# Kernel tuning notes

Hardware: AMD Instinct MI355X
Metric: run time of the kernel (lower is better)

## Reference

```python
import jax, jax.numpy as jnp
import numpy as np

B, T, D, H = 8, 2048, 1024, 128  # batch, seq, input_size, head_size


def setup_inputs() -> dict:
    key = jax.random.key(0)
    kx, kq, kk, kv = jax.random.split(key, 4)
    s = 1.0 / np.sqrt(D)
    return {
        "x": jax.random.normal(kx, (B, T, D), dtype=jnp.float32),
        "Wq": jax.random.normal(kq, (D, H), dtype=jnp.float32) * s,
        "Wk": jax.random.normal(kk, (D, H), dtype=jnp.float32) * s,
        "Wv": jax.random.normal(kv, (D, H), dtype=jnp.float32) * s,
    }


def reference(x, Wq, Wk, Wv):
    # projections (Linear, no bias)
    q = jnp.einsum("btd,dh->bth", x, Wq)
    k = jnp.einsum("btd,dh->bth", x, Wk)
    v = jnp.einsum("btd,dh->bth", x, Wv)
    scale = H ** (-0.5)
    scores = jnp.einsum("bth,bsh->bts", q, k) * scale  # [B,T,T]
    t = x.shape[1]
    causal = jnp.tril(jnp.ones((t, t), dtype=bool))
    scores = jnp.where(causal, scores, -jnp.inf)
    attn = jax.nn.softmax(scores, axis=-1)  # dropout p=0.0 -> identity
    out = jnp.einsum("bts,bsh->bth", attn, v)
    return out
```

## Files before the change

### kernel.cpp

```cpp
#include <hip/hip_runtime.h>
#include <math.h>

#define B_ 8
#define T_ 2048
#define D_ 1024
#define H_ 128
#define BT (B_ * T_)

typedef short bf16x8 __attribute__((ext_vector_type(8)));
typedef float f32x4 __attribute__((ext_vector_type(4)));

static constexpr float SCALE = 0.08838834764831845f;

__device__ inline unsigned short f2b(float f) {
  unsigned int u = __float_as_uint(f);
  u += 0x7FFF + ((u >> 16) & 1);
  return (unsigned short)(u >> 16);
}
__device__ inline unsigned int pk2(float a, float b) {
  return (unsigned int)f2b(a) | ((unsigned int)f2b(b) << 16);
}

__device__ __forceinline__ void gll16(const void* g, void* l) {
  __builtin_amdgcn_global_load_lds(
      (const __attribute__((address_space(1))) void*)g,
      (__attribute__((address_space(3))) void*)l, 16, 0, 0);
}

__global__ __launch_bounds__(256) void wcvt_kernel(
    const float* __restrict__ Wq, const float* __restrict__ Wk,
    const float* __restrict__ Wv, short* __restrict__ Wt) {
  __shared__ short Wls[128 * 72];
  const int sel = blockIdx.y;
  const float* W = sel == 0 ? Wq : (sel == 1 ? Wk : Wv);
  const int d0 = blockIdx.x * 64;
  const int tid = threadIdx.x;
#pragma unroll
  for (int i = 0; i < 8; ++i) {
    int slot = tid + i * 256;
    int r = slot >> 5, hg = slot & 31;
    float4 w = *(const float4*)(W + (size_t)(d0 + r) * H_ + hg * 4);
    Wls[(hg * 4 + 0) * 72 + r] = (short)f2b(w.x);
    Wls[(hg * 4 + 1) * 72 + r] = (short)f2b(w.y);
    Wls[(hg * 4 + 2) * 72 + r] = (short)f2b(w.z);
    Wls[(hg * 4 + 3) * 72 + r] = (short)f2b(w.w);
  }
  __syncthreads();
  short* dst = Wt + (size_t)sel * D_ * H_;
#pragma unroll
  for (int i = 0; i < 4; ++i) {
    int slot = tid + i * 256;
    int h = slot >> 3, g = slot & 7;
    *(int4*)(dst + (size_t)h * D_ + d0 + g * 8) = *(int4*)&Wls[h * 72 + g * 8];
  }
}

__global__ __launch_bounds__(256) void proj_kernel(
    const float* __restrict__ x, const short* __restrict__ Wt,
    short* __restrict__ qb, short* __restrict__ kb, short* __restrict__ vtb) {
  __shared__ alignas(16) char smem[49152];
  short* Xs0 = (short*)smem;
  short* Xs1 = (short*)(smem + 8192);
  short* Ws0 = (short*)(smem + 16384);
  short* Ws1 = (short*)(smem + 32768);

  const int tid = threadIdx.x;
  const int wave = tid >> 6, lane = tid & 63;
  const int ln = lane & 15, quad = lane >> 4;
  const int mw = wave & 1, nw = wave >> 1;
  const int sel = blockIdx.y;
  const int row0 = blockIdx.x * 64;
  const short* W = Wt + (size_t)sel * (size_t)(D_ * H_);

  f32x4 acc[2][4];
#pragma unroll
  for (int mi = 0; mi < 2; ++mi)
#pragma unroll
    for (int ni = 0; ni < 4; ++ni) acc[mi][ni] = (f32x4){0.f, 0.f, 0.f, 0.f};

  auto stage = [&](int bf, int k0) {
    short* Ws = bf ? Ws1 : Ws0;
#pragma unroll
    for (int j = 0; j < 4; ++j) {
      const int rbase = wave * 32 + j * 8;
      const int n = rbase + (lane >> 3);
      const int gp = (lane & 7) ^ (n & 7);
      gll16(W + (size_t)n * D_ + k0 + gp * 8, (char*)Ws + rbase * 128);
    }
    short* Xs = bf ? Xs1 : Xs0;
    float4 xr[4];
#pragma unroll
    for (int i = 0; i < 4; ++i) {
      int fid = tid + i * 256;
      int r = fid >> 4, g4 = fid & 15;
      xr[i] = *(const float4*)(x + (size_t)(row0 + r) * D_ + k0 + g4 * 4);
    }
#pragma unroll
    for (int i = 0; i < 4; ++i) {
      int fid = tid + i * 256;
      int r = fid >> 4, g4 = fid & 15;
      int g = g4 >> 1, half = g4 & 1;
      unsigned int* p = (unsigned int*)&Xs[r * 64 + ((g ^ (r & 7)) * 8) + half * 4];
      p[0] = pk2(xr[i].x, xr[i].y);
      p[1] = pk2(xr[i].z, xr[i].w);
    }
  };

  stage(0, 0);
  for (int s = 0; s < 16; ++s) {
    __syncthreads();
    if (s < 15) stage((s + 1) & 1, (s + 1) * 64);
    const short* Xs = (s & 1) ? Xs1 : Xs0;
    const short* Ws = (s & 1) ? Ws1 : Ws0;
#pragma unroll
    for (int kk = 0; kk < 2; ++kk) {
      bf16x8 a[2];
#pragma unroll
      for (int mi = 0; mi < 2; ++mi) {
        int r = mw * 32 + mi * 16 + ln;
        a[mi] = *(bf16x8*)&Xs[r * 64 + (((kk * 4 + quad) ^ (r & 7)) * 8)];
      }
#pragma unroll
      for (int ni = 0; ni < 4; ++ni) {
        int n = nw * 64 + ni * 16 + ln;
        bf16x8 bb = *(bf16x8*)&Ws[n * 64 + (((kk * 4 + quad) ^ (n & 7)) * 8)];
#pragma unroll
        for (int mi = 0; mi < 2; ++mi)
          acc[mi][ni] = __builtin_amdgcn_mfma_f32_16x16x32_bf16(a[mi], bb, acc[mi][ni], 0, 0, 0);
      }
    }
  }

  __syncthreads();
  short* Cs = (short*)smem;
  if (sel < 2) {
    short* out = sel ? kb : qb;
#pragma unroll
    for (int mi = 0; mi < 2; ++mi)
#pragma unroll
      for (int ni = 0; ni < 4; ++ni)
#pragma unroll
        for (int rr = 0; rr < 4; ++rr)
          Cs[(mw * 32 + mi * 16 + quad * 4 + rr) * 136 + nw * 64 + ni * 16 + ln] =
              (short)f2b(acc[mi][ni][rr]);
    __syncthreads();
#pragma unroll
    for (int i = 0; i < 4; ++i) {
      int slot = tid + i * 256;
      int r = slot >> 4, g = slot & 15;
      *(int4*)(out + (size_t)(row0 + r) * H_ + g * 8) = *(int4*)&Cs[r * 136 + g * 8];
    }
  } else {
#pragma unroll
    for (int mi = 0; mi < 2; ++mi)
#pragma unroll
      for (int ni = 0; ni < 4; ++ni)
#pragma unroll
        for (int rr = 0; rr < 4; ++rr)
          Cs[(nw * 64 + ni * 16 + ln) * 72 + mw * 32 + mi * 16 + quad * 4 + rr] =
              (short)f2b(acc[mi][ni][rr]);
    __syncthreads();
    const int b = row0 >> 11, t0 = row0 & 2047;
#pragma unroll
    for (int i = 0; i < 4; ++i) {
      int slot = tid + i * 256;
      int h = slot >> 3, g = slot & 7;
      *(int4*)(vtb + (size_t)(b * H_ + h) * T_ + t0 + g * 8) = *(int4*)&Cs[h * 72 + g * 8];
    }
  }
}

__global__ __launch_bounds__(256) void attn_part(
    const short* __restrict__ qb, const short* __restrict__ kb,
    const short* __restrict__ vtb, float* __restrict__ po,
    float* __restrict__ pm, float* __restrict__ pl) {
  __shared__ alignas(16) char smem[74240];
  short* Ks0 = (short*)smem;
  short* Ks1 = (short*)(smem + 16384);
  short* Vt0 = (short*)(smem + 32768);
  short* Vt1 = (short*)(smem + 49152);
  short* Pt  = (short*)(smem + 65536);

  const int tid = threadIdx.x;
  const int wv = tid >> 6, lane = tid & 63;
  const int ln = lane & 15, quad = lane >> 4;
  const int b = blockIdx.x / 80;
  const int rr = 79 - (blockIdx.x % 80);
  const int g = (rr >= 48) ? 3 : (rr >= 24) ? 2 : (rr >= 8) ? 1 : 0;
  const int local = rr - 4 * g * (g + 1);
  const int j = 8 * g + local / (g + 1);
  const int s = local - (local / (g + 1)) * (g + 1);
  const int sid = b * 80 + rr;
  const int q0 = j * 64;
  const int nchunks = min(8, j + 1 - 8 * s);

  short* myP = Pt + wv * (16 * 68);

  bf16x8 qfr[4];
#pragma unroll
  for (int kk = 0; kk < 4; ++kk)
    qfr[kk] = *(const bf16x8*)(qb + (size_t)(b * T_ + q0 + wv * 16 + ln) * H_ +
                               kk * 32 + quad * 8);

  f32x4 oacc[8];
#pragma unroll
  for (int ht = 0; ht < 8; ++ht) oacc[ht] = (f32x4){0.f, 0.f, 0.f, 0.f};

  float m_run = -INFINITY, l_run = 0.f;
  const int qglob = q0 + wv * 16 + ln;

  auto stageK = [&](short* dst, int s0) {
#pragma unroll
    for (int jj = 0; jj < 4; ++jj) {
      const int rb = wv * 16 + jj * 4;
      const int r = rb + (lane >> 4);
      const int gp = (lane & 15) ^ (r & 7);
      gll16(kb + (size_t)(b * T_ + s0 + r) * H_ + gp * 8, (char*)dst + rb * 256);
    }
  };
  auto stageV = [&](short* dst, int s0) {
#pragma unroll
    for (int jj = 0; jj < 4; ++jj) {
      const int hb = wv * 32 + jj * 8;
      const int h = hb + (lane >> 3);
      const int gp = (lane & 7) ^ (h & 7);
      gll16(vtb + (size_t)(b * H_ + h) * T_ + s0 + gp * 8, (char*)dst + hb * 128);
    }
  };

  stageK(Ks0, 8 * s * 64);
  stageV(Vt0, 8 * s * 64);

  for (int ch = 0; ch < nchunks; ++ch) {
    const int s0 = (8 * s + ch) * 64;
    const int cur = ch & 1;
    __syncthreads();
    if (ch + 1 < nchunks) {
      stageK(cur ? Ks0 : Ks1, s0 + 64);
      stageV(cur ? Vt0 : Vt1, s0 + 64);
    }
    const short* Kc = cur ? Ks1 : Ks0;
    const short* Vc = cur ? Vt1 : Vt0;

    f32x4 sacc[4];
#pragma unroll
    for (int t = 0; t < 4; ++t) sacc[t] = (f32x4){0.f, 0.f, 0.f, 0.f};
#pragma unroll
    for (int kk = 0; kk < 4; ++kk) {
#pragma unroll
      for (int t = 0; t < 4; ++t) {
        const int krow = t * 16 + ln;
        bf16x8 kf = *(bf16x8*)&Kc[krow * 128 + (((kk * 4 + quad) ^ (ln & 7)) * 8)];
        sacc[t] = __builtin_amdgcn_mfma_f32_16x16x32_bf16(kf, qfr[kk], sacc[t], 0, 0, 0);
      }
    }

    float sv[4][4];
    float mc = -INFINITY;
#pragma unroll
    for (int t = 0; t < 4; ++t)
#pragma unroll
      for (int r = 0; r < 4; ++r) {
        const int key = s0 + t * 16 + quad * 4 + r;
        float sc = sacc[t][r] * SCALE;
        sv[t][r] = (key <= qglob) ? sc : -INFINITY;
        mc = fmaxf(mc, sv[t][r]);
      }
    mc = fmaxf(mc, __shfl_xor(mc, 16));
    mc = fmaxf(mc, __shfl_xor(mc, 32));
    const float mnew = fmaxf(m_run, mc);
    const float alpha = __expf(m_run - mnew);
    float lc = 0.f;
    float p[4][4];
#pragma unroll
    for (int t = 0; t < 4; ++t)
#pragma unroll
      for (int r = 0; r < 4; ++r) {
        p[t][r] = __expf(sv[t][r] - mnew);
        lc += p[t][r];
      }
    lc += __shfl_xor(lc, 16);
    lc += __shfl_xor(lc, 32);
    l_run = l_run * alpha + lc;
    m_run = mnew;

#pragma unroll
    for (int t = 0; t < 4; ++t) {
      *(unsigned int*)&myP[ln * 68 + t * 16 + quad * 4 + 0] = pk2(p[t][0], p[t][1]);
      *(unsigned int*)&myP[ln * 68 + t * 16 + quad * 4 + 2] = pk2(p[t][2], p[t][3]);
    }
#pragma unroll
    for (int ht = 0; ht < 8; ++ht)
#pragma unroll
      for (int r = 0; r < 4; ++r) oacc[ht][r] *= alpha;

#pragma unroll
    for (int kk2 = 0; kk2 < 2; ++kk2) {
      bf16x8 pf = *(bf16x8*)&myP[ln * 68 + kk2 * 32 + quad * 8];
#pragma unroll
      for (int ht = 0; ht < 8; ++ht) {
        const int hrow = ht * 16 + ln;
        bf16x8 vf = *(bf16x8*)&Vc[hrow * 64 + (((kk2 * 4 + quad) ^ (ln & 7)) * 8)];
        oacc[ht] = __builtin_amdgcn_mfma_f32_16x16x32_bf16(vf, pf, oacc[ht], 0, 0, 0);
      }
    }
  }

  if (quad == 0) {
    pm[(size_t)sid * 64 + wv * 16 + ln] = m_run;
    pl[(size_t)sid * 64 + wv * 16 + ln] = l_run;
  }
  __syncthreads();
  float* Ot = (float*)smem;
#pragma unroll
  for (int ht = 0; ht < 8; ++ht)
    *(f32x4*)&Ot[(wv * 16 + ln) * 132 + ht * 16 + quad * 4] = oacc[ht];
  __syncthreads();
  float* dst = po + (size_t)sid * 8192;
#pragma unroll
  for (int i = 0; i < 8; ++i) {
    int slot2 = tid + i * 256;
    int r2 = slot2 >> 5, c2 = slot2 & 31;
    *(f32x4*)(dst + r2 * 128 + c2 * 4) = *(f32x4*)&Ot[r2 * 132 + c2 * 4];
  }
}

__global__ __launch_bounds__(256) void attn_reduce(
    const float* __restrict__ po, const float* __restrict__ pm,
    const float* __restrict__ pl, float* __restrict__ out) {
  const int b = blockIdx.x >> 5;
  const int j = blockIdx.x & 31;
  const int g = j >> 3;
  const int nseg = g + 1;
  const int sid0 = b * 80 + 4 * g * (g + 1) + (j - 8 * g) * nseg;
  const int tid = threadIdx.x;
  const int q = tid >> 2, hq = tid & 3;

  float m[4], l[4], a[4];
  float M = -INFINITY;
  for (int s2 = 0; s2 < nseg; ++s2) {
    m[s2] = pm[(size_t)(sid0 + s2) * 64 + q];
    l[s2] = pl[(size_t)(sid0 + s2) * 64 + q];
    M = fmaxf(M, m[s2]);
  }
  float lsum = 0.f;
  for (int s2 = 0; s2 < nseg; ++s2) {
    a[s2] = __expf(m[s2] - M);
    lsum += a[s2] * l[s2];
  }
  f32x4 acc[8];
#pragma unroll
  for (int i = 0; i < 8; ++i) acc[i] = (f32x4){0.f, 0.f, 0.f, 0.f};
  for (int s2 = 0; s2 < nseg; ++s2) {
    const float* src = po + (size_t)(sid0 + s2) * 8192 + q * 128 + hq * 32;
    const float as = a[s2];
#pragma unroll
    for (int i = 0; i < 8; ++i) {
      f32x4 v = *(const f32x4*)(src + i * 4);
#pragma unroll
      for (int c = 0; c < 4; ++c) acc[i][c] += as * v[c];
    }
  }
  const float inv = 1.0f / lsum;
  float* o = out + ((size_t)(b * T_ + j * 64 + q)) * H_ + hq * 32;
#pragma unroll
  for (int i = 0; i < 8; ++i) {
    f32x4 v;
#pragma unroll
    for (int c = 0; c < 4; ++c) v[c] = acc[i][c] * inv;
    *(f32x4*)(o + i * 4) = v;
  }
}

extern "C" void kernel_launch(void* const* d_in, const int* in_sizes, int n_in,
                              void* d_out, int out_size, void* d_ws, size_t ws_size,
                              hipStream_t stream) {
  const float* x  = (const float*)d_in[0];
  const float* Wq = (const float*)d_in[1];
  const float* Wk = (const float*)d_in[2];
  const float* Wv = (const float*)d_in[3];
  float* out = (float*)d_out;

  char* ws = (char*)d_ws;
  short* qb  = (short*)(ws);
  short* kb  = (short*)(ws + 4194304);
  short* vtb = (short*)(ws + 8388608);
  short* Wt  = (short*)(ws + 12582912);
  float* po  = (float*)(ws + 14680064);
  float* pm  = (float*)(ws + 35651584);
  float* pl  = (float*)(ws + 35915776);

  wcvt_kernel<<<dim3(D_ / 64, 3), 256, 0, stream>>>(Wq, Wk, Wv, Wt);
  proj_kernel<<<dim3(BT / 64, 3), 256, 0, stream>>>(x, Wt, qb, kb, vtb);
  attn_part<<<dim3(8 * 80), 256, 0, stream>>>(qb, kb, vtb, po, pm, pl);
  attn_reduce<<<dim3(8 * 32), 256, 0, stream>>>(po, pm, pl, out);
}
```

Before: 165.4 us.

## Load K/V fragments directly from global memory and drop LDS staging in attention

Removes the double-buffered LDS staging of K and V tiles and has each wave read its MFMA operands straight from global memory, relying on L1/L2 for reuse across waves. It also reorders block indexing so batches interleave, skips the causal mask on fully-unmasked chunks, and writes partial outputs directly without an LDS transpose. The aim is to cut LDS footprint and barriers to raise occupancy. The cost is more redundant global/L2 traffic and less coalesced access (the V reads are strided by T).

```diff
diff --git a/kernel.cpp b/kernel.cpp
--- a/kernel.cpp
+++ b/kernel.cpp
@@ -174,18 +174,13 @@
     const short* __restrict__ qb, const short* __restrict__ kb,
     const short* __restrict__ vtb, float* __restrict__ po,
     float* __restrict__ pm, float* __restrict__ pl) {
-  __shared__ alignas(16) char smem[74240];
-  short* Ks0 = (short*)smem;
-  short* Ks1 = (short*)(smem + 16384);
-  short* Vt0 = (short*)(smem + 32768);
-  short* Vt1 = (short*)(smem + 49152);
-  short* Pt  = (short*)(smem + 65536);
+  __shared__ short Pt[4 * 16 * 68];
 
   const int tid = threadIdx.x;
   const int wv = tid >> 6, lane = tid & 63;
   const int ln = lane & 15, quad = lane >> 4;
-  const int b = blockIdx.x / 80;
-  const int rr = 79 - (blockIdx.x % 80);
+  const int b = blockIdx.x & 7;
+  const int rr = 79 - (blockIdx.x >> 3);
   const int g = (rr >= 48) ? 3 : (rr >= 24) ? 2 : (rr >= 8) ? 1 : 0;
   const int local = rr - 4 * g * (g + 1);
   const int j = 8 * g + local / (g + 1);
@@ -195,6 +190,9 @@
   const int nchunks = min(8, j + 1 - 8 * s);
 
   short* myP = Pt + wv * (16 * 68);
+  const int qglob = q0 + wv * 16 + ln;
+  const short* Kbase = kb + (size_t)b * T_ * H_;
+  const short* Vbase = vtb + (size_t)b * H_ * T_;
 
   bf16x8 qfr[4];
 #pragma unroll
@@ -207,65 +205,46 @@
   for (int ht = 0; ht < 8; ++ht) oacc[ht] = (f32x4){0.f, 0.f, 0.f, 0.f};
 
   float m_run = -INFINITY, l_run = 0.f;
-  const int qglob = q0 + wv * 16 + ln;
-
-  auto stageK = [&](short* dst, int s0) {
-#pragma unroll
-    for (int jj = 0; jj < 4; ++jj) {
-      const int rb = wv * 16 + jj * 4;
-      const int r = rb + (lane >> 4);
-      const int gp = (lane & 15) ^ (r & 7);
-      gll16(kb + (size_t)(b * T_ + s0 + r) * H_ + gp * 8, (char*)dst + rb * 256);
-    }
-  };
-  auto stageV = [&](short* dst, int s0) {
-#pragma unroll
-    for (int jj = 0; jj < 4; ++jj) {
-      const int hb = wv * 32 + jj * 8;
-      const int h = hb + (lane >> 3);
-      const int gp = (lane & 7) ^ (h & 7);
-      gll16(vtb + (size_t)(b * H_ + h) * T_ + s0 + gp * 8, (char*)dst + hb * 128);
-    }
-  };
-
-  stageK(Ks0, 8 * s * 64);
-  stageV(Vt0, 8 * s * 64);
 
   for (int ch = 0; ch < nchunks; ++ch) {
     const int s0 = (8 * s + ch) * 64;
-    const int cur = ch & 1;
-    __syncthreads();
-    if (ch + 1 < nchunks) {
-      stageK(cur ? Ks0 : Ks1, s0 + 64);
-      stageV(cur ? Vt0 : Vt1, s0 + 64);
-    }
-    const short* Kc = cur ? Ks1 : Ks0;
-    const short* Vc = cur ? Vt1 : Vt0;
 
     f32x4 sacc[4];
 #pragma unroll
     for (int t = 0; t < 4; ++t) sacc[t] = (f32x4){0.f, 0.f, 0.f, 0.f};
 #pragma unroll
     for (int kk = 0; kk < 4; ++kk) {
-#pragma unroll
-      for (int t = 0; t < 4; ++t) {
-        const int krow = t * 16 + ln;
-        bf16x8 kf = *(bf16x8*)&Kc[krow * 128 + (((kk * 4 + quad) ^ (ln & 7)) * 8)];
-        sacc[t] = __builtin_amdgcn_mfma_f32_16x16x32_bf16(kf, qfr[kk], sacc[t], 0, 0, 0);
-      }
+      bf16x8 kf[4];
+#pragma unroll
+      for (int t = 0; t < 4; ++t)
+        kf[t] = *(const bf16x8*)(Kbase + (size_t)(s0 + t * 16 + ln) * H_ +
+                                 kk * 32 + quad * 8);
+#pragma unroll
+      for (int t = 0; t < 4; ++t)
+        sacc[t] = __builtin_amdgcn_mfma_f32_16x16x32_bf16(kf[t], qfr[kk], sacc[t], 0, 0, 0);
     }
 
     float sv[4][4];
     float mc = -INFINITY;
-#pragma unroll
-    for (int t = 0; t < 4; ++t)
-#pragma unroll
-      for (int r = 0; r < 4; ++r) {
-        const int key = s0 + t * 16 + quad * 4 + r;
-        float sc = sacc[t][r] * SCALE;
-        sv[t][r] = (key <= qglob) ? sc : -INFINITY;
-        mc = fmaxf(mc, sv[t][r]);
-      }
+    if (s0 + 63 <= q0 + wv * 16) {
+#pragma unroll
+      for (int t = 0; t < 4; ++t)
+#pragma unroll
+        for (int r = 0; r < 4; ++r) {
+          sv[t][r] = sacc[t][r] * SCALE;
+          mc = fmaxf(mc, sv[t][r]);
+        }
+    } else {
+#pragma unroll
+      for (int t = 0; t < 4; ++t)
+#pragma unroll
+        for (int r = 0; r < 4; ++r) {
+          const int key = s0 + t * 16 + quad * 4 + r;
+          float sc = sacc[t][r] * SCALE;
+          sv[t][r] = (key <= qglob) ? sc : -INFINITY;
+          mc = fmaxf(mc, sv[t][r]);
+        }
+    }
     mc = fmaxf(mc, __shfl_xor(mc, 16));
     mc = fmaxf(mc, __shfl_xor(mc, 32));
     const float mnew = fmaxf(m_run, mc);
@@ -299,8 +278,8 @@
       bf16x8 pf = *(bf16x8*)&myP[ln * 68 + kk2 * 32 + quad * 8];
 #pragma unroll
       for (int ht = 0; ht < 8; ++ht) {
-        const int hrow = ht * 16 + ln;
-        bf16x8 vf = *(bf16x8*)&Vc[hrow * 64 + (((kk2 * 4 + quad) ^ (ln & 7)) * 8)];
+        bf16x8 vf = *(const bf16x8*)(Vbase + (size_t)(ht * 16 + ln) * T_ +
+                                     s0 + kk2 * 32 + quad * 8);
         oacc[ht] = __builtin_amdgcn_mfma_f32_16x16x32_bf16(vf, pf, oacc[ht], 0, 0, 0);
       }
     }
@@ -310,19 +289,10 @@
     pm[(size_t)sid * 64 + wv * 16 + ln] = m_run;
     pl[(size_t)sid * 64 + wv * 16 + ln] = l_run;
   }
-  __syncthreads();
-  float* Ot = (float*)smem;
+  float* dst = po + (size_t)sid * 8192 + (size_t)(wv * 16 + ln) * 128;
 #pragma unroll
   for (int ht = 0; ht < 8; ++ht)
-    *(f32x4*)&Ot[(wv * 16 + ln) * 132 + ht * 16 + quad * 4] = oacc[ht];
-  __syncthreads();
-  float* dst = po + (size_t)sid * 8192;
-#pragma unroll
-  for (int i = 0; i < 8; ++i) {
-    int slot2 = tid + i * 256;
-    int r2 = slot2 >> 5, c2 = slot2 & 31;
-    *(f32x4*)(dst + r2 * 128 + c2 * 4) = *(f32x4*)&Ot[r2 * 132 + c2 * 4];
-  }
+    *(f32x4*)(dst + ht * 16 + quad * 4) = oacc[ht];
 }
 
 __global__ __launch_bounds__(256) void attn_reduce(
```

New measurement: 218.5 us. 1.32x slower.

## Halve attention KV chunk to 32 keys for higher occupancy, add lazy rescale

Applied to the files above, without the earlier changes.

The attention partial kernel now stages 32-key K/V chunks instead of 64. This halves shared memory to about 37KB, and launch bounds request 4 blocks per SM to raise occupancy. The change also skips causal masking on fully unmasked chunks and only rescales the accumulator when the running max grows by more than a threshold. Block-to-batch mapping is interleaved across batches. In exchange there are twice as many sync and staging iterations, plus a new V swizzle pattern.

```diff
diff --git a/kernel.cpp b/kernel.cpp
--- a/kernel.cpp
+++ b/kernel.cpp
@@ -170,31 +170,32 @@
   }
 }
 
-__global__ __launch_bounds__(256) void attn_part(
+__global__ __launch_bounds__(256, 4) void attn_part(
     const short* __restrict__ qb, const short* __restrict__ kb,
     const short* __restrict__ vtb, float* __restrict__ po,
     float* __restrict__ pm, float* __restrict__ pl) {
-  __shared__ alignas(16) char smem[74240];
+  __shared__ alignas(16) char smem[37376];
   short* Ks0 = (short*)smem;
-  short* Ks1 = (short*)(smem + 16384);
-  short* Vt0 = (short*)(smem + 32768);
-  short* Vt1 = (short*)(smem + 49152);
-  short* Pt  = (short*)(smem + 65536);
+  short* Ks1 = (short*)(smem + 8192);
+  short* Vt0 = (short*)(smem + 16384);
+  short* Vt1 = (short*)(smem + 24576);
+  short* Pt  = (short*)(smem + 32768);
 
   const int tid = threadIdx.x;
   const int wv = tid >> 6, lane = tid & 63;
   const int ln = lane & 15, quad = lane >> 4;
-  const int b = blockIdx.x / 80;
-  const int rr = 79 - (blockIdx.x % 80);
+  const int b = blockIdx.x & 7;
+  const int rr = 79 - (blockIdx.x >> 3);
   const int g = (rr >= 48) ? 3 : (rr >= 24) ? 2 : (rr >= 8) ? 1 : 0;
   const int local = rr - 4 * g * (g + 1);
   const int j = 8 * g + local / (g + 1);
   const int s = local - (local / (g + 1)) * (g + 1);
   const int sid = b * 80 + rr;
   const int q0 = j * 64;
-  const int nchunks = min(8, j + 1 - 8 * s);
-
-  short* myP = Pt + wv * (16 * 68);
+  const int nchunks = min(16, 2 * (j + 1) - 16 * s);
+
+  short* myP = Pt + wv * (16 * 36);
+  const int qglob = q0 + wv * 16 + ln;
 
   bf16x8 qfr[4];
 #pragma unroll
@@ -207,12 +208,11 @@
   for (int ht = 0; ht < 8; ++ht) oacc[ht] = (f32x4){0.f, 0.f, 0.f, 0.f};
 
   float m_run = -INFINITY, l_run = 0.f;
-  const int qglob = q0 + wv * 16 + ln;
 
   auto stageK = [&](short* dst, int s0) {
 #pragma unroll
-    for (int jj = 0; jj < 4; ++jj) {
-      const int rb = wv * 16 + jj * 4;
+    for (int jj = 0; jj < 2; ++jj) {
+      const int rb = wv * 8 + jj * 4;
       const int r = rb + (lane >> 4);
       const int gp = (lane & 15) ^ (r & 7);
       gll16(kb + (size_t)(b * T_ + s0 + r) * H_ + gp * 8, (char*)dst + rb * 256);
@@ -220,89 +220,101 @@
   };
   auto stageV = [&](short* dst, int s0) {
 #pragma unroll
-    for (int jj = 0; jj < 4; ++jj) {
-      const int hb = wv * 32 + jj * 8;
-      const int h = hb + (lane >> 3);
-      const int gp = (lane & 7) ^ (h & 7);
-      gll16(vtb + (size_t)(b * H_ + h) * T_ + s0 + gp * 8, (char*)dst + hb * 128);
+    for (int jj = 0; jj < 2; ++jj) {
+      const int hb = wv * 32 + jj * 16;
+      const int h = hb + (lane >> 2);
+      const int gp = (lane & 3) ^ (h & 3) ^ ((h >> 2) & 3);
+      gll16(vtb + (size_t)(b * H_ + h) * T_ + s0 + gp * 8, (char*)dst + hb * 64);
     }
   };
 
-  stageK(Ks0, 8 * s * 64);
-  stageV(Vt0, 8 * s * 64);
+  stageK(Ks0, 512 * s);
+  stageV(Vt0, 512 * s);
 
   for (int ch = 0; ch < nchunks; ++ch) {
-    const int s0 = (8 * s + ch) * 64;
+    const int s0 = 512 * s + ch * 32;
     const int cur = ch & 1;
     __syncthreads();
     if (ch + 1 < nchunks) {
-      stageK(cur ? Ks0 : Ks1, s0 + 64);
-      stageV(cur ? Vt0 : Vt1, s0 + 64);
+      stageK(cur ? Ks0 : Ks1, s0 + 32);
+      stageV(cur ? Vt0 : Vt1, s0 + 32);
     }
     const short* Kc = cur ? Ks1 : Ks0;
     const short* Vc = cur ? Vt1 : Vt0;
 
-    f32x4 sacc[4];
-#pragma unroll
-    for (int t = 0; t < 4; ++t) sacc[t] = (f32x4){0.f, 0.f, 0.f, 0.f};
+    f32x4 sacc[2];
+#pragma unroll
+    for (int t = 0; t < 2; ++t) sacc[t] = (f32x4){0.f, 0.f, 0.f, 0.f};
 #pragma unroll
     for (int kk = 0; kk < 4; ++kk) {
 #pragma unroll
-      for (int t = 0; t < 4; ++t) {
+      for (int t = 0; t < 2; ++t) {
         const int krow = t * 16 + ln;
-        bf16x8 kf = *(bf16x8*)&Kc[krow * 128 + (((kk * 4 + quad) ^ (ln & 7)) * 8)];
+        bf16x8 kf = *(bf16x8*)&Kc[krow * 128 + (((kk * 4 + quad) ^ (krow & 7)) * 8)];
         sacc[t] = __builtin_amdgcn_mfma_f32_16x16x32_bf16(kf, qfr[kk], sacc[t], 0, 0, 0);
       }
     }
 
-    float sv[4][4];
+    float sv[2][4];
     float mc = -INFINITY;
-#pragma unroll
-    for (int t = 0; t < 4; ++t)
-#pragma unroll
-      for (int r = 0; r < 4; ++r) {
-        const int key = s0 + t * 16 + quad * 4 + r;
-        float sc = sacc[t][r] * SCALE;
-        sv[t][r] = (key <= qglob) ? sc : -INFINITY;
-        mc = fmaxf(mc, sv[t][r]);
-      }
+    if (s0 + 31 <= q0 + wv * 16) {
+#pragma unroll
+      for (int t = 0; t < 2; ++t)
+#pragma unroll
+        for (int r = 0; r < 4; ++r) {
+          sv[t][r] = sacc[t][r] * SCALE;
+          mc = fmaxf(mc, sv[t][r]);
+        }
+    } else {
+#pragma unroll
+      for (int t = 0; t < 2; ++t)
+#pragma unroll
+        for (int r = 0; r < 4; ++r) {
+          const int key = s0 + t * 16 + quad * 4 + r;
+          float sc = sacc[t][r] * SCALE;
+          sv[t][r] = (key <= qglob) ? sc : -INFINITY;
+          mc = fmaxf(mc, sv[t][r]);
+        }
+    }
     mc = fmaxf(mc, __shfl_xor(mc, 16));
     mc = fmaxf(mc, __shfl_xor(mc, 32));
-    const float mnew = fmaxf(m_run, mc);
-    const float alpha = __expf(m_run - mnew);
+
+    if (!__all(mc <= m_run + 8.f)) {
+      const float mnew = fmaxf(m_run, mc);
+      const float alpha = __expf(m_run - mnew);
+#pragma unroll
+      for (int ht = 0; ht < 8; ++ht)
+#pragma unroll
+        for (int r = 0; r < 4; ++r) oacc[ht][r] *= alpha;
+      l_run *= alpha;
+      m_run = mnew;
+    }
     float lc = 0.f;
-    float p[4][4];
-#pragma unroll
-    for (int t = 0; t < 4; ++t)
+    float p[2][4];
+#pragma unroll
+    for (int t = 0; t < 2; ++t)
 #pragma unroll
       for (int r = 0; r < 4; ++r) {
-        p[t][r] = __expf(sv[t][r] - mnew);
+        p[t][r] = __expf(sv[t][r] - m_run);
         lc += p[t][r];
       }
     lc += __shfl_xor(lc, 16);
     lc += __shfl_xor(lc, 32);
-    l_run = l_run * alpha + lc;
-    m_run = mnew;
-
-#pragma unroll
-    for (int t = 0; t < 4; ++t) {
-      *(unsigned int*)&myP[ln * 68 + t * 16 + quad * 4 + 0] = pk2(p[t][0], p[t][1]);
-      *(unsigned int*)&myP[ln * 68 + t * 16 + quad * 4 + 2] = pk2(p[t][2], p[t][3]);
-    }
-#pragma unroll
-    for (int ht = 0; ht < 8; ++ht)
-#pragma unroll
-      for (int r = 0; r < 4; ++r) oacc[ht][r] *= alpha;
-
-#pragma unroll
-    for (int kk2 = 0; kk2 < 2; ++kk2) {
-      bf16x8 pf = *(bf16x8*)&myP[ln * 68 + kk2 * 32 + quad * 8];
-#pragma unroll
-      for (int ht = 0; ht < 8; ++ht) {
-        const int hrow = ht * 16 + ln;
-        bf16x8 vf = *(bf16x8*)&Vc[hrow * 64 + (((kk2 * 4 + quad) ^ (ln & 7)) * 8)];
-        oacc[ht] = __builtin_amdgcn_mfma_f32_16x16x32_bf16(vf, pf, oacc[ht], 0, 0, 0);
-      }
+    l_run += lc;
+
+#pragma unroll
+    for (int t = 0; t < 2; ++t) {
+      *(unsigned int*)&myP[ln * 36 + t * 16 + quad * 4 + 0] = pk2(p[t][0], p[t][1]);
+      *(unsigned int*)&myP[ln * 36 + t * 16 + quad * 4 + 2] = pk2(p[t][2], p[t][3]);
+    }
+
+    bf16x8 pf = *(bf16x8*)&myP[ln * 36 + quad * 8];
+#pragma unroll
+    for (int ht = 0; ht < 8; ++ht) {
+      const int hrow = ht * 16 + ln;
+      const int slot = quad ^ (hrow & 3) ^ ((hrow >> 2) & 3);
+      bf16x8 vf = *(bf16x8*)&Vc[hrow * 32 + slot * 8];
+      oacc[ht] = __builtin_amdgcn_mfma_f32_16x16x32_bf16(vf, pf, oacc[ht], 0, 0, 0);
     }
   }
 
```

Measured after the change: 158.0 us. -4.5%, faster.
